# Kernel optimization log

Hardware: AMD Instinct MI355X
Metric: run time of the kernel (lower is better)

The kernel has to match this reference:

```python
import jax, jax.numpy as jnp
import numpy as np
import math

HEADS, LANDMARKS, PINV_ITERS, RES_K = 8, 256, 6, 33
DIM = 512


def layer_norm(x, g, b, eps=1e-5):
    mu = x.mean(-1, keepdims=True)
    var = ((x - mu) ** 2).mean(-1, keepdims=True)
    return (x - mu) * jax.lax.rsqrt(var + eps) * g + b


def iter_pinv(x, iters=PINV_ITERS):
    # Moore-Penrose pseudo-inverse via Newton-Schulz-like iteration (lucidrains nystrom-attention)
    ax = jnp.abs(x)
    z = jnp.swapaxes(x, -1, -2) / (jnp.max(ax.sum(-1)) * jnp.max(ax.sum(-2)))
    I = jnp.eye(x.shape[-1], dtype=x.dtype)
    for _ in range(iters):
        xz = x @ z
        z = 0.25 * z @ (13.0 * I - xz @ (15.0 * I - xz @ (7.0 * I - xz)))
    return z


def nystrom_attention(x, qkv_w, out_w, out_b, res_w):
    b, n, dim = x.shape
    h, m = HEADS, LANDMARKS
    d = dim // h
    pad = (m - n % m) % m
    xp = jnp.pad(x, ((0, 0), (pad, 0), (0, 0)))  # pad at sequence start (as in original)
    npad = n + pad
    qkv = xp @ qkv_w  # [b, npad, 3*dim]
    q, k, v = jnp.split(qkv, 3, axis=-1)
    q, k, v = (t.reshape(b, npad, h, d).transpose(0, 2, 1, 3) for t in (q, k, v))
    q = q * (d ** -0.5)
    l = npad // m
    q_l = q.reshape(b, h, m, l, d).mean(3)  # [b,h,m,d] landmarks
    k_l = k.reshape(b, h, m, l, d).mean(3)
    attn1 = jax.nn.softmax(jnp.einsum('bhid,bhjd->bhij', q, k_l), axis=-1)    # [b,h,npad,m]
    attn2 = jax.nn.softmax(jnp.einsum('bhid,bhjd->bhij', q_l, k_l), axis=-1)  # [b,h,m,m]
    attn3 = jax.nn.softmax(jnp.einsum('bhid,bhjd->bhij', q_l, k), axis=-1)    # [b,h,m,npad]
    out = (attn1 @ iter_pinv(attn2)) @ (attn3 @ v)  # [b,h,npad,d]
    # depthwise residual conv over sequence dim: v as NCHW = [b, heads, npad, d], kernel (33,1)
    res = jax.lax.conv_general_dilated(
        v, res_w, window_strides=(1, 1), padding=((RES_K // 2, RES_K // 2), (0, 0)),
        dimension_numbers=('NCHW', 'OIHW', 'NCHW'), feature_group_count=h)
    out = out + res
    out = out.transpose(0, 2, 1, 3).reshape(b, npad, dim)
    out = out @ out_w + out_b  # dropout is identity at eval
    return out[:, -n:]


def dwconv(x, w, b, k):
    y = jax.lax.conv_general_dilated(
        x, w, (1, 1), ((k // 2, k // 2), (k // 2, k // 2)),
        dimension_numbers=('NCHW', 'OIHW', 'NCHW'), feature_group_count=x.shape[1])
    return y + b[None, :, None, None]


def ppeg(x, H, W, w7, b7, w5, b5, w3, b3):
    B, _, C = x.shape
    cls_tok, feat = x[:, :1], x[:, 1:]
    cnn = feat.transpose(0, 2, 1).reshape(B, C, H, W)
    y = cnn + dwconv(cnn, w7, b7, 7) + dwconv(cnn, w5, b5, 5) + dwconv(cnn, w3, b3, 3)
    y = y.reshape(B, C, H * W).transpose(0, 2, 1)
    return jnp.concatenate([cls_tok, y], axis=1)


def _forward(features, fc1_w, fc1_b, cls_token,
             l1_norm_g, l1_norm_b, l1_qkv_w, l1_out_w, l1_out_b, l1_res_w,
             ppeg_w7, ppeg_b7, ppeg_w5, ppeg_b5, ppeg_w3, ppeg_b3,
             l2_norm_g, l2_norm_b, l2_qkv_w, l2_out_w, l2_out_b, l2_res_w,
             norm_g, norm_b, fc2_w, fc2_b):
    h = jax.nn.relu(features @ fc1_w + fc1_b)  # [B, N, 512]
    B, N, D = h.shape
    _H = _W = int(math.ceil(math.sqrt(N)))
    add_length = _H * _W - N
    h = jnp.concatenate([h, h[:, :add_length, :]], axis=1)  # square pad by wraparound
    h = jnp.concatenate([jnp.broadcast_to(cls_token, (B, 1, D)), h], axis=1)
    h = h + nystrom_attention(layer_norm(h, l1_norm_g, l1_norm_b), l1_qkv_w, l1_out_w, l1_out_b, l1_res_w)
    h = ppeg(h, _H, _W, ppeg_w7, ppeg_b7, ppeg_w5, ppeg_b5, ppeg_w3, ppeg_b3)
    h = h + nystrom_attention(layer_norm(h, l2_norm_g, l2_norm_b), l2_qkv_w, l2_out_w, l2_out_b, l2_res_w)
    h = layer_norm(h, norm_g, norm_b)[:, 0]
    return h @ fc2_w + fc2_b  # [B, num_classes]


def setup_inputs() -> dict:
    key = jax.random.key(0)
    ks = jax.random.split(key, 32)
    B, N, F, D = 2, 16000, 1024, DIM
    s = 0.02
    def rn(k, shape, scale=s):
        return jax.random.normal(k, shape, dtype=jnp.float32) * scale
    inp = {
        'features': jax.random.normal(ks[0], (B, N, F), dtype=jnp.float32),
        'fc1_w': rn(ks[1], (F, D)), 'fc1_b': jnp.zeros((D,), jnp.float32),
        'cls_token': rn(ks[2], (1, 1, D), 1.0),
        'l1_norm_g': jnp.ones((D,), jnp.float32), 'l1_norm_b': jnp.zeros((D,), jnp.float32),
        'l1_qkv_w': rn(ks[3], (D, 3 * D)),
        'l1_out_w': rn(ks[4], (D, D)), 'l1_out_b': jnp.zeros((D,), jnp.float32),
        'l1_res_w': rn(ks[5], (HEADS, 1, RES_K, 1)),
        'ppeg_w7': rn(ks[6], (D, 1, 7, 7)), 'ppeg_b7': jnp.zeros((D,), jnp.float32),
        'ppeg_w5': rn(ks[7], (D, 1, 5, 5)), 'ppeg_b5': jnp.zeros((D,), jnp.float32),
        'ppeg_w3': rn(ks[8], (D, 1, 3, 3)), 'ppeg_b3': jnp.zeros((D,), jnp.float32),
        'l2_norm_g': jnp.ones((D,), jnp.float32), 'l2_norm_b': jnp.zeros((D,), jnp.float32),
        'l2_qkv_w': rn(ks[9], (D, 3 * D)),
        'l2_out_w': rn(ks[10], (D, D)), 'l2_out_b': jnp.zeros((D,), jnp.float32),
        'l2_res_w': rn(ks[11], (HEADS, 1, RES_K, 1)),
        'norm_g': jnp.ones((D,), jnp.float32), 'norm_b': jnp.zeros((D,), jnp.float32),
        'fc2_w': rn(ks[12], (D, 1)), 'fc2_b': jnp.zeros((1,), jnp.float32),
    }
    return inp


def reference(features, fc1_w, fc1_b, cls_token,
              l1_norm_g, l1_norm_b, l1_qkv_w, l1_out_w, l1_out_b, l1_res_w,
              ppeg_w7, ppeg_b7, ppeg_w5, ppeg_b5, ppeg_w3, ppeg_b3,
              l2_norm_g, l2_norm_b, l2_qkv_w, l2_out_w, l2_out_b, l2_res_w,
              norm_g, norm_b, fc2_w, fc2_b):
    return _forward(features, fc1_w, fc1_b, cls_token,
                    l1_norm_g, l1_norm_b, l1_qkv_w, l1_out_w, l1_out_b, l1_res_w,
                    ppeg_w7, ppeg_b7, ppeg_w5, ppeg_b5, ppeg_w3, ppeg_b3,
                    l2_norm_g, l2_norm_b, l2_qkv_w, l2_out_w, l2_out_b, l2_res_w,
                    norm_g, norm_b, fc2_w, fc2_b)
```

## Files before the change

### kernel.cpp

```cpp
#include <hip/hip_runtime.h>
#include <math.h>

#define NTOK 16130
#define NPAD 16384
#define PADF 254
#define NB   2
#define DM   512
#define NH   8
#define HD   64
#define LM   256
#define SEG  64

typedef __attribute__((ext_vector_type(8))) short short8v;
typedef __attribute__((ext_vector_type(4))) float f32x4;
typedef unsigned int u32;

__device__ __forceinline__ float wred_max(float v){
  #pragma unroll
  for(int o=32;o;o>>=1) v=fmaxf(v,__shfl_xor(v,o));
  return v;
}
__device__ __forceinline__ float wred_sum(float v){
  #pragma unroll
  for(int o=32;o;o>>=1) v+=__shfl_xor(v,o);
  return v;
}
__device__ __forceinline__ float block_max256(float v, float* s4){
  v=wred_max(v);
  if((threadIdx.x&63)==0) s4[threadIdx.x>>6]=v;
  __syncthreads();
  v=fmaxf(fmaxf(s4[0],s4[1]),fmaxf(s4[2],s4[3]));
  __syncthreads();
  return v;
}
__device__ __forceinline__ float block_sum256(float v, float* s4){
  v=wred_sum(v);
  if((threadIdx.x&63)==0) s4[threadIdx.x>>6]=v;
  __syncthreads();
  v=s4[0]+s4[1]+s4[2]+s4[3];
  __syncthreads();
  return v;
}
__device__ __forceinline__ unsigned short f2bf(float f){
  unsigned u=__float_as_uint(f);
  u = u + 0x7FFFu + ((u>>16)&1u);
  return (unsigned short)(u>>16);
}
__device__ __forceinline__ float bf2f(unsigned short u){
  return __uint_as_float(((unsigned)u)<<16);
}
__device__ __forceinline__ unsigned cvtpk(float a, float b){
  unsigned r;
  asm("v_cvt_pk_bf16_f32 %0, %1, %2" : "=v"(r) : "v"(a), "v"(b));
  return r;
}
__device__ __forceinline__ void gl16(const unsigned short* g, unsigned short* l){
  __builtin_amdgcn_global_load_lds(
      (const __attribute__((address_space(1))) u32*)(g),
      (__attribute__((address_space(3))) u32*)(l), 16, 0, 0);
}

__global__ void k_f2bf4(const float* __restrict__ x, unsigned short* __restrict__ y, int n4){
  int i=blockIdx.x*256+threadIdx.x; if(i>=n4) return;
  float4 v=((const float4*)x)[i];
  ushort4 r; r.x=f2bf(v.x); r.y=f2bf(v.y); r.z=f2bf(v.z); r.w=f2bf(v.w);
  ((ushort4*)y)[i]=r;
}
__global__ void k_wconv_t(const float* __restrict__ W, unsigned short* __restrict__ Wt,
                          int K, int N){
  int idx=blockIdx.x*256+threadIdx.x; if(idx>=K*N) return;
  int k=idx/N, n=idx%N;
  Wt[(size_t)n*K+k]=f2bf(W[idx]);
}

template<int MODE, int ASRC>
__global__ __launch_bounds__(256) void k_mfma_gemm(
    const void* __restrict__ Ap, const unsigned short* __restrict__ Bt,
    int M, int N, int K,
    const float* __restrict__ bias,
    void* __restrict__ o0, void* __restrict__ o1, void* __restrict__ o2)
{
  __shared__ __align__(16) unsigned short Sh[128*64];
  int t=threadIdx.x;
  int bx=blockIdx.x, by=blockIdx.y;
  {
    int gx=gridDim.x; int wg=by*gx+bx; int nwg=gx*gridDim.y;
    int cpx=nwg>>3; int x2=(wg&7)*cpx+(wg>>3);
    by=x2/gx; bx=x2-by*gx;
  }
  int row0=by*128, col0=bx*128;
  int lane=t&63, w=t>>6, wr=w>>1, wc=w&1, lr=lane&15, kg=lane>>4;
  f32x4 acc[4][4];
  #pragma unroll
  for(int m=0;m<4;m++)
    #pragma unroll
    for(int n=0;n<4;n++) acc[m][n]=(f32x4){0.f,0.f,0.f,0.f};

  for(int k0=0;k0<K;k0+=32){
    __syncthreads();
    #pragma unroll
    for(int i=0;i<2;i++){
      int flat=i*256+t, r=flat>>2, k8=flat&3;
      int kofs=k0+k8*8;
      const unsigned short* asrc;
      if constexpr(ASRC==0){
        asrc=(const unsigned short*)Ap+(size_t)(row0+r)*K+kofs;
      } else {
        int rr2=row0+r; int bb=rr2>>14, ri=rr2&16383;
        int head=kofs>>6, dd=kofs&63;
        asrc=(const unsigned short*)Ap + (((size_t)bb*NH+head)*NPAD+ri)*HD + dd;
      }
      gl16(asrc, Sh+(size_t)flat*8);
      gl16(Bt+(size_t)(col0+r)*K+kofs, Sh+4096+(size_t)flat*8);
    }
    __syncthreads();
    short8v af[4], bf[4];
    #pragma unroll
    for(int m=0;m<4;m++) af[m]=*(const short8v*)(Sh+(wr*64+m*16+lr)*32 + kg*8);
    #pragma unroll
    for(int n=0;n<4;n++) bf[n]=*(const short8v*)(Sh+4096+(wc*64+n*16+lr)*32 + kg*8);
    #pragma unroll
    for(int m=0;m<4;m++)
      #pragma unroll
      for(int n=0;n<4;n++)
        acc[m][n]=__builtin_amdgcn_mfma_f32_16x16x32_bf16(af[m],bf[n],acc[m][n],0,0,0);
  }
  if constexpr(MODE==1){
    #pragma unroll
    for(int p=0;p<2;p++){
      __syncthreads();
      #pragma unroll
      for(int mm=0;mm<2;mm++){
        int m=2*p+mm;
        #pragma unroll
        for(int n=0;n<4;n++){
          int cc=wc*64+n*16+lr;
          int c=col0+cc;
          float sc=((c>>9)==0)?0.125f:1.f;
          #pragma unroll
          for(int j=0;j<4;j++){
            int lrow=wr*32+mm*16+kg*4+j;
            Sh[lrow*128+cc]=f2bf(acc[m][n][j]*sc);
          }
        }
      }
      __syncthreads();
      #pragma unroll
      for(int i=0;i<4;i++){
        int p2=i*256+t;
        int r2=p2>>4, ck=p2&15;
        int grow=row0+(r2>>5)*64+(2*p+((r2>>4)&1))*16+(r2&15);
        int bb=grow>>14, rr=grow&16383;
        int c=col0+ck*8;
        int which=c>>9, hcol=c&511, head=hcol>>6, dd=hcol&63;
        unsigned short* dst=(which==0)?(unsigned short*)o0:
                            (which==1)?(unsigned short*)o1:(unsigned short*)o2;
        *(short8v*)(dst + (((size_t)bb*NH+head)*NPAD+rr)*HD+dd) =
            *(const short8v*)(Sh + r2*128 + ck*8);
      }
    }
  } else {
    #pragma unroll
    for(int m=0;m<4;m++){
      int rbase=row0 + wr*64 + m*16 + kg*4;
      #pragma unroll
      for(int j=0;j<4;j++){
        int r=rbase+j;
        #pragma unroll
        for(int n=0;n<4;n++){
          int c=col0 + wc*64 + n*16 + lr;
          float val=acc[m][n][j];
          if(MODE==0){
            float* h=(float*)o0;
            int bb=(r>=16000)?1:0, ii=r-bb*16000;
            float vv=fmaxf(val+bias[c],0.f);
            h[((size_t)bb*NTOK + 1 + ii)*DM + c]=vv;
            if(ii<129) h[((size_t)bb*NTOK + 16001 + ii)*DM + c]=vv;
          } else {
            float* h=(float*)o0;
            int bb=r>>14, rr=r&16383;
            if(rr>=PADF)
              h[((size_t)bb*NTOK + (rr-PADF))*DM + c]+=val+bias[c];
          }
        }
      }
    }
  }
}

__global__ void k_cls(const float* __restrict__ cls, float* __restrict__ h){
  int t=blockIdx.x*256+threadIdx.x;
  if(t<2*DM) h[(size_t)(t>>9)*NTOK*DM + (t&511)]=cls[t&511];
}

__global__ __launch_bounds__(256) void k_lnpad(
    const float* __restrict__ h, const float* __restrict__ g,
    const float* __restrict__ bta, unsigned short* __restrict__ xln)
{
  int r=blockIdx.x;
  int bb=r>>14, i=r&16383;
  int t=threadIdx.x;
  unsigned short* dst=xln+(size_t)r*DM;
  if(i<PADF){ dst[t]=0; dst[t+256]=0; return; }
  const float* src=h+((size_t)bb*NTOK + (i-PADF))*DM;
  float x0=src[t], x1=src[t+256];
  __shared__ float s4[4];
  float mu=block_sum256(x0+x1,s4)*(1.f/512.f);
  float d0=x0-mu, d1=x1-mu;
  float var=block_sum256(d0*d0+d1*d1,s4)*(1.f/512.f);
  float rst=rsqrtf(var+1e-5f);
  dst[t]    =f2bf(d0*rst*g[t]    +bta[t]);
  dst[t+256]=f2bf(d1*rst*g[t+256]+bta[t+256]);
}

__global__ void k_lmean2(const unsigned short* __restrict__ qsrc,
                         const unsigned short* __restrict__ ksrc,
                         float* __restrict__ qlf, unsigned short* __restrict__ qlb_,
                         float* __restrict__ klf, unsigned short* __restrict__ klb_){
  int gid=blockIdx.x;
  const unsigned short* src; float* dstf; unsigned short* dstb;
  if(gid<4096){ src=qsrc; dstf=qlf; dstb=qlb_; }
  else        { src=ksrc; dstf=klf; dstb=klb_; gid-=4096; }
  int bh=gid>>8, s=gid&255, d=threadIdx.x;
  const unsigned short* p=src + (((size_t)bh*NPAD)+s*SEG)*HD + d;
  float acc=0.f;
  #pragma unroll
  for(int l=0;l<SEG;l++) acc+=bf2f(p[(size_t)l*HD]);
  float m=acc*(1.f/64.f);
  dstf[((size_t)bh*LM+s)*HD+d]=m;
  dstb[((size_t)bh*LM+s)*HD+d]=f2bf(m);
}

__global__ __launch_bounds__(256) void k_vtrans(
    const unsigned short* __restrict__ v, unsigned short* __restrict__ vt)
{
  __shared__ unsigned short tile[64][72];
  int kt=blockIdx.x, bh=blockIdx.y;
  int t=threadIdx.x;
  int r=t>>2, sgq=t&3;
  const short8v* src=(const short8v*)(v + ((size_t)bh*NPAD + kt*64 + r)*HD + sgq*16);
  *(short8v*)(&tile[r][sgq*16])  =src[0];
  *(short8v*)(&tile[r][sgq*16+8])=src[1];
  __syncthreads();
  int d=t>>2;
  union{unsigned short u[16]; short8v v8[2];} pk;
  #pragma unroll
  for(int i=0;i<16;i++) pk.u[i]=tile[sgq*16+i][d];
  short8v* dst=(short8v*)(vt + ((size_t)bh*HD + d)*NPAD + kt*64 + sgq*16);
  dst[0]=pk.v8[0]; dst[1]=pk.v8[1];
}

__global__ __launch_bounds__(256) void k_attn2(
    const float* __restrict__ ql, const float* __restrict__ kl,
    float* __restrict__ attn2,
    unsigned short* __restrict__ a2h, unsigned short* __restrict__ a2l)
{
  __shared__ float qrow[64]; __shared__ float s4[4];
  int bh=blockIdx.x>>8, i=blockIdx.x&255, j=threadIdx.x;
  if(j<64) qrow[j]=ql[((size_t)bh*LM+i)*HD+j];
  __syncthreads();
  const float* kp=kl+((size_t)bh*LM+j)*HD;
  float l=0.f;
  #pragma unroll
  for(int d=0;d<64;d++) l+=qrow[d]*kp[d];
  float m=block_max256(l,s4);
  float e=__expf(l-m);
  float s=block_sum256(e,s4);
  float pv=e/s;
  size_t o=((size_t)bh*LM+i)*LM+j;
  attn2[o]=pv;
  unsigned short hh=f2bf(pv);
  a2h[o]=hh; a2l[o]=f2bf(pv-bf2f(hh));
}

__global__ void k_colsum(const float* __restrict__ x, float* __restrict__ cs){
  int bh=blockIdx.x, j=threadIdx.x;
  const float* p=x+(size_t)bh*65536;
  float s=0.f;
  for(int i=0;i<256;i++) s+=p[(size_t)i*256+j];
  cs[bh*256+j]=s;
}
__global__ void k_pinvscale(const float* __restrict__ cs, float* __restrict__ scale){
  __shared__ float s4[4];
  float mc=-1e30f;
  for(int i=threadIdx.x;i<4096;i+=256) mc=fmaxf(mc,cs[i]);
  mc=block_max256(mc,s4);
  if(threadIdx.x==0) scale[0]=1.f/mc;
}
__global__ void k_zinit_hl(const float* __restrict__ x, const float* __restrict__ scale,
    unsigned short* __restrict__ zh, unsigned short* __restrict__ zl,
    unsigned short* __restrict__ zth, unsigned short* __restrict__ ztl){
  int bh=blockIdx.x>>8, i=blockIdx.x&255, j=threadIdx.x;
  float s=scale[0];
  size_t base=(size_t)bh*65536;
  float vn=x[base+(size_t)j*256+i]*s;
  float vt=x[base+(size_t)i*256+j]*s;
  size_t o=base+(size_t)i*256+j;
  unsigned short h=f2bf(vn); zh[o]=h; zl[o]=f2bf(vn-bf2f(h));
  h=f2bf(vt); zth[o]=h; ztl[o]=f2bf(vt-bf2f(h));
}

template<int MODE, int PREC>
__global__ __launch_bounds__(256) void k_bmm3(
    const unsigned short* __restrict__ Ah, const unsigned short* __restrict__ Al,
    const unsigned short* __restrict__ Bth, const unsigned short* __restrict__ Btl,
    const unsigned short* __restrict__ Xh, const unsigned short* __restrict__ Xl,
    unsigned short* __restrict__ Cnh, unsigned short* __restrict__ Cnl,
    unsigned short* __restrict__ Cth, unsigned short* __restrict__ Ctl,
    int Ndim)
{
  __shared__ unsigned short AsH[32*72], BsH[64*72];
  __shared__ unsigned short AsL[PREC?32*72:8], BsL[PREC?64*72:8];
  int bh=blockIdx.z;
  int n0=blockIdx.x*64, m0=blockIdx.y*32;
  int t=threadIdx.x, lane=t&63, w=t>>6;
  int c=lane&15, g=lane>>4;
  int wr=(w>>1)*16, wc=(w&1)*32;
  f32x4 acc[2];
  acc[0]=(f32x4){0.f,0.f,0.f,0.f};
  acc[1]=(f32x4){0.f,0.f,0.f,0.f};
  size_t Abase=(size_t)bh*65536;
  size_t Bbase=(size_t)bh*(size_t)Ndim*256;
  int r=t>>3, k8=(t&7)*8;
  const unsigned short* ApH =Ah +Abase+(size_t)(m0+r)*256+k8;
  const unsigned short* BpH0=Bth+Bbase+(size_t)(n0+r)*256+k8;
  const unsigned short* BpH1=Bth+Bbase+(size_t)(n0+32+r)*256+k8;
  const unsigned short* ApL =Al +Abase+(size_t)(m0+r)*256+k8;
  const unsigned short* BpL0=Btl+Bbase+(size_t)(n0+r)*256+k8;
  const unsigned short* BpL1=Btl+Bbase+(size_t)(n0+32+r)*256+k8;
  short8v rah,rbh0,rbh1, ral,rbl0,rbl1;
  rah =*(const short8v*)(ApH);
  rbh0=*(const short8v*)(BpH0);
  rbh1=*(const short8v*)(BpH1);
  if constexpr(PREC==1){
    ral =*(const short8v*)(ApL);
    rbl0=*(const short8v*)(BpL0);
    rbl1=*(const short8v*)(BpL1);
  }
  int k0=0;
  for(;;){
    __syncthreads();
    *(short8v*)(AsH + r*72 + k8)=rah;
    *(short8v*)(BsH + r*72 + k8)=rbh0;
    *(short8v*)(BsH + (r+32)*72 + k8)=rbh1;
    if constexpr(PREC==1){
      *(short8v*)(AsL + r*72 + k8)=ral;
      *(short8v*)(BsL + r*72 + k8)=rbl0;
      *(short8v*)(BsL + (r+32)*72 + k8)=rbl1;
    }
    __syncthreads();
    int kn=k0+64;
    if(kn<256){
      rah =*(const short8v*)(ApH +kn);
      rbh0=*(const short8v*)(BpH0+kn);
      rbh1=*(const short8v*)(BpH1+kn);
      if constexpr(PREC==1){
        ral =*(const short8v*)(ApL +kn);
        rbl0=*(const short8v*)(BpL0+kn);
        rbl1=*(const short8v*)(BpL1+kn);
      }
    }
    #pragma unroll
    for(int ks=0;ks<2;ks++){
      short8v af=*(const short8v*)(AsH+(wr+c)*72 + ks*32 + g*8);
      short8v alf;
      if constexpr(PREC==1) alf=*(const short8v*)(AsL+(wr+c)*72 + ks*32 + g*8);
      #pragma unroll
      for(int nt=0;nt<2;nt++){
        short8v bf=*(const short8v*)(BsH+(wc+nt*16+c)*72 + ks*32 + g*8);
        acc[nt]=__builtin_amdgcn_mfma_f32_16x16x32_bf16(af,bf,acc[nt],0,0,0);
        if constexpr(PREC==1){
          short8v blf=*(const short8v*)(BsL+(wc+nt*16+c)*72 + ks*32 + g*8);
          acc[nt]=__builtin_amdgcn_mfma_f32_16x16x32_bf16(af,blf,acc[nt],0,0,0);
          acc[nt]=__builtin_amdgcn_mfma_f32_16x16x32_bf16(alf,bf,acc[nt],0,0,0);
        }
      }
    }
    if(kn>=256) break;
    k0=kn;
  }
  int rb=m0+wr+g*4;
  #pragma unroll
  for(int nt=0;nt<2;nt++){
    int cc=n0+wc+nt*16+c;
    float vv[4];
    #pragma unroll
    for(int j=0;j<4;j++){
      float a=acc[nt][j];
      int rr=rb+j;
      if(MODE==1){
        float xv=bf2f(Xh[Abase+(size_t)rr*256+cc])+bf2f(Xl[Abase+(size_t)rr*256+cc]);
        a=(rr==cc?15.f:0.f)-7.f*xv+a;
      } else if(MODE==2){
        a=(rr==cc?13.f:0.f)-a;
      } else if(MODE==3){
        a*=0.25f;
      }
      vv[j]=a;
    }
    if(MODE==0||MODE==3){
      #pragma unroll
      for(int j=0;j<4;j++){
        unsigned short hh=f2bf(vv[j]);
        Cnh[Abase+(size_t)(rb+j)*256+cc]=hh;
        Cnl[Abase+(size_t)(rb+j)*256+cc]=f2bf(vv[j]-bf2f(hh));
      }
    }
    {
      ushort4 hv, lv;
      hv.x=f2bf(vv[0]); hv.y=f2bf(vv[1]); hv.z=f2bf(vv[2]); hv.w=f2bf(vv[3]);
      lv.x=f2bf(vv[0]-bf2f(hv.x)); lv.y=f2bf(vv[1]-bf2f(hv.y));
      lv.z=f2bf(vv[2]-bf2f(hv.z)); lv.w=f2bf(vv[3]-bf2f(hv.w));
      size_t co=((size_t)bh*Ndim+cc)*256+rb;
      *(ushort4*)(Cth+co)=hv;
      if(MODE!=4) *(ushort4*)(Ctl+co)=lv;
    }
  }
}

__global__ __launch_bounds__(512) void k_attn3m(
    const unsigned short* __restrict__ qlb,
    const unsigned short* __restrict__ kb,
    const unsigned short* __restrict__ vtb,
    float* __restrict__ pacc, float* __restrict__ pms)
{
  __shared__ unsigned short Ks[64*72];
  __shared__ unsigned short Vs[64*72];
  int ck=blockIdx.x, rh=blockIdx.y, bh=blockIdx.z;
  int t=threadIdx.x, lane=t&63, w=t>>6;
  int c=lane&15, g=lane>>4;
  int qrow0=rh*128 + w*16;
  short8v Qf[2];
  #pragma unroll
  for(int kw=0;kw<2;kw++)
    Qf[kw]=*(const short8v*)(qlb + ((size_t)bh*LM + qrow0 + c)*HD + kw*32 + g*8);
  f32x4 accO[4];
  float mrun=-3e38f, srun=0.f;
  #pragma unroll
  for(int d=0;d<4;d++) accO[d]=(f32x4){0.f,0.f,0.f,0.f};
  int sr=t>>3, sgk=t&7;
  for(int sc=0;sc<16;++sc){
    int key0=ck*1024 + sc*64;
    __syncthreads();
    *(short8v*)(Ks + sr*72 + sgk*8) =
      *(const short8v*)(kb + ((size_t)bh*NPAD + key0 + sr)*HD + sgk*8);
    *(short8v*)(Vs + sr*72 + sgk*8) =
      *(const short8v*)(vtb + ((size_t)bh*HD + sr)*NPAD + key0 + sgk*8);
    __syncthreads();
    f32x4 s[4];
    #pragma unroll
    for(int mt=0;mt<4;mt++){
      short8v a0=*(const short8v*)(Ks + (mt*16+c)*72 + g*8);
      short8v a1=*(const short8v*)(Ks + (mt*16+c)*72 + 32 + g*8);
      f32x4 z=(f32x4){0.f,0.f,0.f,0.f};
      z=__builtin_amdgcn_mfma_f32_16x16x32_bf16(a0,Qf[0],z,0,0,0);
      z=__builtin_amdgcn_mfma_f32_16x16x32_bf16(a1,Qf[1],z,0,0,0);
      s[mt]=z;
    }
    unsigned U[4][2];
    {
      float cm=-3e38f;
      #pragma unroll
      for(int mt=0;mt<4;mt++)
        #pragma unroll
        for(int j=0;j<4;j++) cm=fmaxf(cm,s[mt][j]);
      cm=fmaxf(cm,__shfl_xor(cm,16));
      cm=fmaxf(cm,__shfl_xor(cm,32));
      float mnew=fmaxf(mrun,cm);
      float f=__expf(mrun-mnew);
      mrun=mnew;
      float ps=0.f;
      #pragma unroll
      for(int mt=0;mt<4;mt++){
        float p0=__expf(s[mt][0]-mnew);
        float p1=__expf(s[mt][1]-mnew);
        float p2=__expf(s[mt][2]-mnew);
        float p3=__expf(s[mt][3]-mnew);
        ps+=p0+p1+p2+p3;
        U[mt][0]=cvtpk(p0,p1);
        U[mt][1]=cvtpk(p2,p3);
      }
      ps+=__shfl_xor(ps,16); ps+=__shfl_xor(ps,32);
      srun=srun*f+ps;
      #pragma unroll
      for(int d=0;d<4;d++){
        accO[d][0]*=f; accO[d][1]*=f; accO[d][2]*=f; accO[d][3]*=f;
      }
    }
    #pragma unroll
    for(int kw=0;kw<2;kw++){
      union{unsigned u[4]; short8v v;} pk;
      #pragma unroll
      for(int wd=0;wd<4;wd++){
        int sl=c+16*(((g&1)<<1)+(wd>>1));
        unsigned va=(unsigned)__shfl((int)U[kw*2  ][wd&1],sl);
        unsigned vb=(unsigned)__shfl((int)U[kw*2+1][wd&1],sl);
        pk.u[wd]=(lane>=32)?vb:va;
      }
      #pragma unroll
      for(int d=0;d<4;d++){
        short8v vf=*(const short8v*)(Vs + (d*16+c)*72 + kw*32 + g*8);
        accO[d]=__builtin_amdgcn_mfma_f32_16x16x32_bf16(vf,pk.v,accO[d],0,0,0);
      }
    }
  }
  size_t pb=((size_t)bh*16+ck)*LM;
  int q=qrow0+c;
  #pragma unroll
  for(int d=0;d<4;d++)
    *(f32x4*)(pacc + (pb+q)*HD + d*16 + g*4)=accO[d];
  if(g==0){ pms[(pb+q)*2]=mrun; pms[(pb+q)*2+1]=srun; }
}
__global__ __launch_bounds__(256) void k_attn3vc(
    const float* __restrict__ pacc, const float* __restrict__ pms,
    unsigned short* __restrict__ a3vth, unsigned short* __restrict__ a3vtl)
{
  int gid=blockIdx.x*4+(threadIdx.x>>6);
  int bh=gid>>8, row=gid&255, lane=threadIdx.x&63;
  float M=-3e38f;
  float ms[16], ss[16];
  #pragma unroll
  for(int c=0;c<16;c++){
    size_t pb=((size_t)bh*16+c)*LM+row;
    ms[c]=pms[pb*2]; ss[c]=pms[pb*2+1];
    M=fmaxf(M,ms[c]);
  }
  float S=0.f,a=0.f;
  #pragma unroll
  for(int c=0;c<16;c++){
    float f=__expf(ms[c]-M);
    S+=ss[c]*f;
    a+=pacc[(((size_t)bh*16+c)*LM+row)*HD+lane]*f;
  }
  float v=a/S;
  unsigned short hi=f2bf(v);
  a3vth[((size_t)bh*HD+lane)*LM+row]=hi;
  a3vtl[((size_t)bh*HD+lane)*LM+row]=f2bf(v-bf2f(hi));
}

__global__ __launch_bounds__(512) void k_attn1m(
    const unsigned short* __restrict__ qb,
    const unsigned short* __restrict__ klb,
    const unsigned short* __restrict__ w2t,
    unsigned short* __restrict__ aohb)
{
  __shared__ unsigned short klS[256*72];
  __shared__ unsigned short w2S[64*264];
  int qt=blockIdx.x, bh=blockIdx.y;
  int t=threadIdx.x, lane=t&63, w=t>>6;
  int c=lane&15, g=lane>>4;
  {
    int r=t>>1, hf=t&1;
    const short8v* s=(const short8v*)(klb + ((size_t)bh*LM+r)*HD + hf*32);
    short8v* d=(short8v*)(klS + r*72 + hf*32);
    d[0]=s[0]; d[1]=s[1]; d[2]=s[2]; d[3]=s[3];
    int r2=t>>3, sg2=t&7;
    const short8v* s2=(const short8v*)(w2t + ((size_t)bh*HD+r2)*LM + sg2*32);
    short8v* d2=(short8v*)(w2S + r2*264 + sg2*32);
    d2[0]=s2[0]; d2[1]=s2[1]; d2[2]=s2[2]; d2[3]=s2[3];
  }
  __syncthreads();
  int q0=qt*256 + w*32;
  #pragma unroll
  for(int n=0;n<2;n++){
    const unsigned short* qrow=qb + ((size_t)bh*NPAD + q0 + n*16 + c)*HD;
    short8v qf0=*(const short8v*)(qrow + g*8);
    short8v qf1=*(const short8v*)(qrow + 32 + g*8);
    f32x4 s[16];
    #pragma unroll
    for(int mt=0;mt<16;mt++){
      short8v a0=*(const short8v*)(klS + (mt*16+c)*72 + g*8);
      short8v a1=*(const short8v*)(klS + (mt*16+c)*72 + 32 + g*8);
      f32x4 z=(f32x4){0.f,0.f,0.f,0.f};
      z=__builtin_amdgcn_mfma_f32_16x16x32_bf16(a0,qf0,z,0,0,0);
      z=__builtin_amdgcn_mfma_f32_16x16x32_bf16(a1,qf1,z,0,0,0);
      s[mt]=z;
    }
    float M=-3e38f;
    #pragma unroll
    for(int mt=0;mt<16;mt++)
      #pragma unroll
      for(int j=0;j<4;j++) M=fmaxf(M,s[mt][j]);
    M=fmaxf(M,__shfl_xor(M,16));
    M=fmaxf(M,__shfl_xor(M,32));
    float sum=0.f;
    unsigned U[16][2];
    #pragma unroll
    for(int mt=0;mt<16;mt++){
      float p0=__expf(s[mt][0]-M);
      float p1=__expf(s[mt][1]-M);
      float p2=__expf(s[mt][2]-M);
      float p3=__expf(s[mt][3]-M);
      sum+=p0+p1+p2+p3;
      U[mt][0]=cvtpk(p0,p1);
      U[mt][1]=cvtpk(p2,p3);
    }
    sum+=__shfl_xor(sum,16); sum+=__shfl_xor(sum,32);
    float inv=1.f/sum;
    f32x4 accO[4];
    #pragma unroll
    for(int d=0;d<4;d++) accO[d]=(f32x4){0.f,0.f,0.f,0.f};
    #pragma unroll
    for(int kw=0;kw<8;kw++){
      union{unsigned u[4]; short8v v;} pk;
      #pragma unroll
      for(int wd=0;wd<4;wd++){
        int sl=c+16*(((g&1)<<1)+(wd>>1));
        unsigned va=(unsigned)__shfl((int)U[kw*2  ][wd&1],sl);
        unsigned vb=(unsigned)__shfl((int)U[kw*2+1][wd&1],sl);
        pk.u[wd]=(lane>=32)?vb:va;
      }
      #pragma unroll
      for(int d=0;d<4;d++){
        short8v vf=*(const short8v*)(w2S + (d*16+c)*264 + kw*32 + g*8);
        accO[d]=__builtin_amdgcn_mfma_f32_16x16x32_bf16(vf,pk.v,accO[d],0,0,0);
      }
    }
    int q=q0+n*16+c;
    #pragma unroll
    for(int d=0;d<4;d++){
      f32x4 o=accO[d];
      uint2 pk2;
      pk2.x=cvtpk(o[0]*inv, o[1]*inv);
      pk2.y=cvtpk(o[2]*inv, o[3]*inv);
      *(uint2*)(aohb + ((size_t)bh*NPAD+q)*HD + d*16 + g*4)=pk2;
    }
  }
}

__global__ __launch_bounds__(256) void k_resconv2(
    const unsigned short* __restrict__ vt, const float* __restrict__ rw,
    unsigned short* __restrict__ aohb){
  int bx=blockIdx.x, bh=blockIdx.y;
  int t=threadIdx.x, d=t&63, g=t>>6;
  int i0=bx*32+g*8;
  int hh=bh&7;
  const unsigned short* vr=vt + ((size_t)bh*HD + d)*NPAD;
  float wv[40];
  int start=i0-16;
  if(start>=0 && start+40<=NPAD){
    #pragma unroll
    for(int b=0;b<5;b++){
      short8v v8=*(const short8v*)(vr+start+b*8);
      #pragma unroll
      for(int j=0;j<8;j++) wv[b*8+j]=bf2f((unsigned short)v8[j]);
    }
  } else {
    #pragma unroll
    for(int t2=0;t2<40;t2++){
      int src=start+t2;
      wv[t2]=(src>=0&&src<NPAD)?bf2f(vr[src]):0.f;
    }
  }
  const float* wt=rw+hh*33;
  #pragma unroll
  for(int p=0;p<8;p++){
    float a=0.f;
    #pragma unroll
    for(int tk=0;tk<33;tk++) a+=wv[p+tk]*wt[tk];
    size_t o=((size_t)bh*NPAD+i0+p)*HD+d;
    aohb[o]=f2bf(bf2f(aohb[o])+a);
  }
}

__global__ void k_wprep(const float* __restrict__ w7, const float* __restrict__ b7,
                        const float* __restrict__ w5, const float* __restrict__ b5,
                        const float* __restrict__ w3, const float* __restrict__ b3,
                        unsigned short* __restrict__ wcat){
  int t=blockIdx.x*256+threadIdx.x;
  if(t>=50*512) return;
  int r=t>>9, c=t&511;
  float v;
  if(r<49){
    int ky=r/7, kx=r%7;
    v=w7[(size_t)c*49+r];
    if(ky>=1&&ky<=5&&kx>=1&&kx<=5) v+=w5[(size_t)c*25+(ky-1)*5+(kx-1)];
    if(ky>=2&&ky<=4&&kx>=2&&kx<=4) v+=w3[(size_t)c*9+(ky-2)*3+(kx-2)];
  } else {
    v=b7[c]+b5[c]+b3[c];
  }
  wcat[t]=f2bf(v);
}

__global__ __launch_bounds__(256,4) void k_ppeg4(
    const float* __restrict__ src, const unsigned short* __restrict__ wcat,
    float* __restrict__ dst)
{
  __shared__ float patch[196][32];
  __shared__ float wsf[50][32];
  int bx=blockIdx.x;
  int cz=blockIdx.y, bb=blockIdx.z;
  int t=threadIdx.x, c=t&31, g=t>>5;
  int ty0=(bx>>4)*8, tx0=(bx&15)*8;
  const float* base=src+((size_t)bb*NTOK+1)*DM + cz*32 + c;
  #pragma unroll
  for(int i=0;i<25;i++){
    int p=g+8*i;
    if(p<196){
      int py=p/14, px=p%14;
      int yy=ty0-3+py, xx=tx0-3+px;
      float v=0.f;
      if(yy>=0&&yy<127&&xx>=0&&xx<127) v=base[(size_t)(yy*127+xx)*DM];
      patch[p][c]=v;
    }
  }
  #pragma unroll
  for(int i=0;i<7;i++){
    int r=g+8*i; if(r<50) wsf[r][c]=bf2f(wcat[(size_t)r*DM + cz*32 + c]);
  }
  __syncthreads();
  float acc[8];
  float bias=wsf[49][c];
  #pragma unroll
  for(int j=0;j<8;j++) acc[j]=patch[(g+3)*14+(j+3)][c]+bias;
  #pragma unroll
  for(int ky=0;ky<7;ky++){
    float win[14];
    #pragma unroll
    for(int x=0;x<14;x++) win[x]=patch[(g+ky)*14+x][c];
    #pragma unroll
    for(int kx=0;kx<7;kx++){
      float wv=wsf[ky*7+kx][c];
      #pragma unroll
      for(int j=0;j<8;j++) acc[j]+=win[j+kx]*wv;
    }
  }
  int y=ty0+g;
  if(y<127){
    #pragma unroll
    for(int j=0;j<8;j++){
      int x=tx0+j;
      if(x<127)
        dst[((size_t)bb*NTOK+1+(size_t)(y*127+x))*DM + cz*32 + c]=acc[j];
    }
  }
}

__global__ void k_cpcls(const float* __restrict__ h, float* __restrict__ dst){
  int t=blockIdx.x*256+threadIdx.x;
  if(t<2*DM) dst[(size_t)(t>>9)*NTOK*DM + (t&511)]=h[(size_t)(t>>9)*NTOK*DM + (t&511)];
}

__global__ __launch_bounds__(256) void k_final(
    const float* __restrict__ h, const float* __restrict__ g, const float* __restrict__ bta,
    const float* __restrict__ w, const float* __restrict__ fb, float* __restrict__ out)
{
  int bb=blockIdx.x, t=threadIdx.x;
  const float* src=h+(size_t)bb*NTOK*DM;
  float x0=src[t], x1=src[t+256];
  __shared__ float s4[4];
  float mu=block_sum256(x0+x1,s4)*(1.f/512.f);
  float d0=x0-mu, d1=x1-mu;
  float var=block_sum256(d0*d0+d1*d1,s4)*(1.f/512.f);
  float rst=rsqrtf(var+1e-5f);
  float y0=d0*rst*g[t]+bta[t], y1=d1*rst*g[t+256]+bta[t+256];
  float dot=block_sum256(y0*w[t]+y1*w[t+256],s4);
  if(t==0) out[bb]=dot+fb[0];
}

extern "C" void kernel_launch(void* const* d_in, const int* in_sizes, int n_in,
                              void* d_out, int out_size, void* d_ws, size_t ws_size,
                              hipStream_t stream){
  (void)in_sizes; (void)n_in; (void)out_size; (void)ws_size;
  const float* features=(const float*)d_in[0];
  const float* fc1_w  =(const float*)d_in[1];
  const float* fc1_b  =(const float*)d_in[2];
  const float* cls_tok=(const float*)d_in[3];
  const float* fc2_w  =(const float*)d_in[24];
  const float* fc2_b  =(const float*)d_in[25];
  float* out=(float*)d_out;

  char* wp=(char*)d_ws;
  auto allocB=[&](size_t bytes)->char*{
    char* p=wp; wp+=((bytes+255)/256)*256; return p;
  };
  float* h    =(float*)allocB((size_t)NB*NTOK*DM*4);
  float* h2   =(float*)allocB((size_t)NB*NTOK*DM*4);
  unsigned short* vb  =(unsigned short*)allocB((size_t)NB*NPAD*DM*2);
  unsigned short* xlnb=(unsigned short*)allocB((size_t)NB*NPAD*DM*2);
  unsigned short* qb  =(unsigned short*)allocB((size_t)NB*NPAD*DM*2);
  unsigned short* kb  =(unsigned short*)allocB((size_t)NB*NPAD*DM*2);
  unsigned short* vtb =(unsigned short*)allocB((size_t)NB*NPAD*DM*2);
  unsigned short* aohb=(unsigned short*)allocB((size_t)NB*NPAD*DM*2);
  unsigned short* wtf=(unsigned short*)allocB((size_t)512*1024*2);
  unsigned short* wtq=(unsigned short*)allocB((size_t)1536*512*2);
  unsigned short* wtp=(unsigned short*)allocB((size_t)512*512*2);
  float* ql =(float*)allocB((size_t)16*LM*HD*4);
  float* kl =(float*)allocB((size_t)16*LM*HD*4);
  unsigned short* qlb=(unsigned short*)allocB((size_t)16*LM*HD*2);
  unsigned short* klb=(unsigned short*)allocB((size_t)16*LM*HD*2);
  float* attn2=(float*)allocB((size_t)16*LM*LM*4);
  unsigned short* a2h=(unsigned short*)allocB((size_t)16*LM*LM*2);
  unsigned short* a2l=(unsigned short*)allocB((size_t)16*LM*LM*2);
  unsigned short* zb[8];
  for(int i=0;i<8;i++) zb[i]=(unsigned short*)allocB((size_t)16*LM*LM*2);
  unsigned short* Abh=(unsigned short*)allocB((size_t)16*LM*LM*2);
  unsigned short* Abl=(unsigned short*)allocB((size_t)16*LM*LM*2);
  unsigned short* Abth=(unsigned short*)allocB((size_t)16*LM*LM*2);
  unsigned short* Abtl=(unsigned short*)allocB((size_t)16*LM*LM*2);
  unsigned short* Ubth=(unsigned short*)allocB((size_t)16*LM*LM*2);
  unsigned short* Ubtl=(unsigned short*)allocB((size_t)16*LM*LM*2);
  unsigned short* Tbth=(unsigned short*)allocB((size_t)16*LM*LM*2);
  unsigned short* Tbtl=(unsigned short*)allocB((size_t)16*LM*LM*2);
  unsigned short* a3vth=(unsigned short*)allocB((size_t)16*HD*LM*2);
  unsigned short* a3vtl=(unsigned short*)allocB((size_t)16*HD*LM*2);
  unsigned short* w2t=(unsigned short*)allocB((size_t)16*HD*LM*2);
  float* pacc=(float*)allocB((size_t)16*16*LM*HD*4);
  float* pms =(float*)allocB((size_t)16*16*LM*2*4);
  float* cs  =(float*)allocB(4096*4);
  float* scl =(float*)allocB(64*4);

  auto nystrom=[&](float* hbuf, const float* ng, const float* nbias, const float* qkvw,
                   const float* outw, const float* outb, const float* resw){
    k_lnpad<<<NB*NPAD,256,0,stream>>>(hbuf, ng, nbias, xlnb);
    k_wconv_t<<<(512*1536+255)/256,256,0,stream>>>(qkvw, wtq, 512, 1536);
    k_mfma_gemm<1,0><<<dim3(12,256),256,0,stream>>>(xlnb, wtq, 32768,1536,512,
                                                    nullptr, qb, kb, vb);
    k_lmean2<<<8192,64,0,stream>>>(qb, kb, ql, qlb, kl, klb);
    k_vtrans<<<dim3(256,16),256,0,stream>>>(vb, vtb);
    k_attn2<<<4096,256,0,stream>>>(ql, kl, attn2, a2h, a2l);
    k_colsum<<<16,256,0,stream>>>(attn2, cs);
    k_pinvscale<<<1,256,0,stream>>>(cs, scl);
    k_zinit_hl<<<4096,256,0,stream>>>(attn2, scl, zb[0],zb[1],zb[2],zb[3]);
    unsigned short *zch=zb[0],*zcl=zb[1],*zcth=zb[2],*zctl=zb[3];
    unsigned short *znh=zb[4],*znl=zb[5],*znth=zb[6],*zntl=zb[7];
    for(int it=0;it<6;it++){
      if(it<5){
        k_bmm3<0,0><<<dim3(4,8,16),256,0,stream>>>(a2h,a2l, zcth,zctl, nullptr,nullptr,
                                                   Abh,Abl, Abth,Abtl, 256);
        k_bmm3<1,0><<<dim3(4,8,16),256,0,stream>>>(Abh,Abl, Abth,Abtl, Abh,Abl,
                                                   nullptr,nullptr, Ubth,Ubtl, 256);
        k_bmm3<2,0><<<dim3(4,8,16),256,0,stream>>>(Abh,Abl, Ubth,Ubtl, nullptr,nullptr,
                                                   nullptr,nullptr, Tbth,Tbtl, 256);
        k_bmm3<3,0><<<dim3(4,8,16),256,0,stream>>>(zch,zcl, Tbth,Tbtl, nullptr,nullptr,
                                                   znh,znl, znth,zntl, 256);
      } else {
        k_bmm3<0,1><<<dim3(4,8,16),256,0,stream>>>(a2h,a2l, zcth,zctl, nullptr,nullptr,
                                                   Abh,Abl, Abth,Abtl, 256);
        k_bmm3<1,1><<<dim3(4,8,16),256,0,stream>>>(Abh,Abl, Abth,Abtl, Abh,Abl,
                                                   nullptr,nullptr, Ubth,Ubtl, 256);
        k_bmm3<2,1><<<dim3(4,8,16),256,0,stream>>>(Abh,Abl, Ubth,Ubtl, nullptr,nullptr,
                                                   nullptr,nullptr, Tbth,Tbtl, 256);
        k_bmm3<3,1><<<dim3(4,8,16),256,0,stream>>>(zch,zcl, Tbth,Tbtl, nullptr,nullptr,
                                                   znh,znl, znth,zntl, 256);
      }
      unsigned short* tp;
      tp=zch; zch=znh; znh=tp;  tp=zcl; zcl=znl; znl=tp;
      tp=zcth; zcth=znth; znth=tp;  tp=zctl; zctl=zntl; zntl=tp;
    }
    k_attn3m<<<dim3(16,2,16),512,0,stream>>>(qlb, kb, vtb, pacc, pms);
    k_attn3vc<<<1024,256,0,stream>>>(pacc, pms, a3vth, a3vtl);
    k_bmm3<4,1><<<dim3(1,8,16),256,0,stream>>>(zch,zcl, a3vth,a3vtl, nullptr,nullptr,
                                               nullptr,nullptr, w2t,nullptr, 64);
    k_attn1m<<<dim3(64,16),512,0,stream>>>(qb, klb, w2t, aohb);
    k_resconv2<<<dim3(512,16),256,0,stream>>>(vtb, resw, aohb);
    k_wconv_t<<<(512*512+255)/256,256,0,stream>>>(outw, wtp, 512, 512);
    k_mfma_gemm<2,3><<<dim3(4,256),256,0,stream>>>(aohb, wtp, 32768,512,512,
                                                   outb, hbuf, nullptr, nullptr);
  };

  unsigned short* featbf=(unsigned short*)h2;
  k_f2bf4<<<32000,256,0,stream>>>(features, featbf, 32000*1024/4);
  k_wconv_t<<<(1024*512+255)/256,256,0,stream>>>(fc1_w, wtf, 1024, 512);
  k_mfma_gemm<0,0><<<dim3(4,250),256,0,stream>>>(featbf, wtf, 32000,512,1024,
                                                 fc1_b, h, nullptr, nullptr);
  k_cls<<<4,256,0,stream>>>(cls_tok, h);

  nystrom(h, (const float*)d_in[4],(const float*)d_in[5],(const float*)d_in[6],
          (const float*)d_in[7],(const float*)d_in[8],(const float*)d_in[9]);

  {
    unsigned short* wcat=(unsigned short*)attn2;
    k_wprep<<<100,256,0,stream>>>(
        (const float*)d_in[10],(const float*)d_in[11],
        (const float*)d_in[12],(const float*)d_in[13],
        (const float*)d_in[14],(const float*)d_in[15], wcat);
    k_cpcls<<<4,256,0,stream>>>(h, h2);
    k_ppeg4<<<dim3(256,16,2),256,0,stream>>>(h, wcat, h2);
  }

  nystrom(h2, (const float*)d_in[16],(const float*)d_in[17],(const float*)d_in[18],
          (const float*)d_in[19],(const float*)d_in[20],(const float*)d_in[21]);

  k_final<<<2,256,0,stream>>>(h2,(const float*)d_in[22],(const float*)d_in[23],
                              fc2_w, fc2_b, out);
}
```

Measured before the change: 1.264 ms.

## Vectorize and tile several small helper kernels for coalesced memory access

The weight transpose-convert kernel and the pinv initialisation now go through a 32x32 shared-memory tile, so both global reads and writes are coalesced and vectorised. LayerNorm-with-padding handles one row per wavefront with float4 loads and wave-shuffle reductions instead of block-wide reductions. The column sum over attn2 is split into two stages so more blocks run in parallel, and it reuses the pacc buffer as scratch. These kernels were strided-access or low-occupancy helpers; the change adds launches and shared-memory syncs in exchange.

```diff
diff --git a/kernel.cpp b/kernel.cpp
--- a/kernel.cpp
+++ b/kernel.cpp
@@ -66,11 +66,18 @@
   ushort4 r; r.x=f2bf(v.x); r.y=f2bf(v.y); r.z=f2bf(v.z); r.w=f2bf(v.w);
   ((ushort4*)y)[i]=r;
 }
-__global__ void k_wconv_t(const float* __restrict__ W, unsigned short* __restrict__ Wt,
-                          int K, int N){
-  int idx=blockIdx.x*256+threadIdx.x; if(idx>=K*N) return;
-  int k=idx/N, n=idx%N;
-  Wt[(size_t)n*K+k]=f2bf(W[idx]);
+__global__ __launch_bounds__(256) void k_wconv_t(
+    const float* __restrict__ W, unsigned short* __restrict__ Wt, int K, int N){
+  __shared__ float T[32][33];
+  int k0=blockIdx.x*32, n0=blockIdx.y*32;
+  int t=threadIdx.x, r=t>>3, c4=(t&7)*4;
+  float4 a=*(const float4*)(W+(size_t)(k0+r)*N + n0+c4);
+  T[r][c4]=a.x; T[r][c4+1]=a.y; T[r][c4+2]=a.z; T[r][c4+3]=a.w;
+  __syncthreads();
+  ushort4 w;
+  w.x=f2bf(T[c4+0][r]); w.y=f2bf(T[c4+1][r]);
+  w.z=f2bf(T[c4+2][r]); w.w=f2bf(T[c4+3][r]);
+  *(ushort4*)(Wt+(size_t)(n0+r)*K + k0+c4)=w;
 }
 
 template<int MODE, int ASRC>
@@ -197,20 +204,37 @@
     const float* __restrict__ h, const float* __restrict__ g,
     const float* __restrict__ bta, unsigned short* __restrict__ xln)
 {
-  int r=blockIdx.x;
-  int bb=r>>14, i=r&16383;
-  int t=threadIdx.x;
-  unsigned short* dst=xln+(size_t)r*DM;
-  if(i<PADF){ dst[t]=0; dst[t+256]=0; return; }
-  const float* src=h+((size_t)bb*NTOK + (i-PADF))*DM;
-  float x0=src[t], x1=src[t+256];
-  __shared__ float s4[4];
-  float mu=block_sum256(x0+x1,s4)*(1.f/512.f);
-  float d0=x0-mu, d1=x1-mu;
-  float var=block_sum256(d0*d0+d1*d1,s4)*(1.f/512.f);
-  float rst=rsqrtf(var+1e-5f);
-  dst[t]    =f2bf(d0*rst*g[t]    +bta[t]);
-  dst[t+256]=f2bf(d1*rst*g[t+256]+bta[t+256]);
+  int wid=blockIdx.x*4+(threadIdx.x>>6);
+  int lane=threadIdx.x&63;
+  int bb=wid>>14, i=wid&16383;
+  unsigned short* dst=xln+(size_t)wid*DM+lane*8;
+  if(i<PADF){
+    ushort4 z=(ushort4){0,0,0,0};
+    *(ushort4*)dst=z; *(ushort4*)(dst+4)=z;
+    return;
+  }
+  const float* src=h+((size_t)bb*NTOK + (i-PADF))*DM + lane*8;
+  float4 v0=*(const float4*)src;
+  float4 v1=*(const float4*)(src+4);
+  float x[8]={v0.x,v0.y,v0.z,v0.w,v1.x,v1.y,v1.z,v1.w};
+  float s=0.f;
+  #pragma unroll
+  for(int k=0;k<8;k++) s+=x[k];
+  float mu=wred_sum(s)*(1.f/512.f);
+  float d[8]; float vs=0.f;
+  #pragma unroll
+  for(int k=0;k<8;k++){ d[k]=x[k]-mu; vs+=d[k]*d[k]; }
+  float rst=rsqrtf(wred_sum(vs)*(1.f/512.f)+1e-5f);
+  float4 g0=*(const float4*)(g+lane*8),   g1=*(const float4*)(g+lane*8+4);
+  float4 b0=*(const float4*)(bta+lane*8), b1=*(const float4*)(bta+lane*8+4);
+  float gg[8]={g0.x,g0.y,g0.z,g0.w,g1.x,g1.y,g1.z,g1.w};
+  float bb8[8]={b0.x,b0.y,b0.z,b0.w,b1.x,b1.y,b1.z,b1.w};
+  ushort4 w0,w1;
+  w0.x=f2bf(d[0]*rst*gg[0]+bb8[0]); w0.y=f2bf(d[1]*rst*gg[1]+bb8[1]);
+  w0.z=f2bf(d[2]*rst*gg[2]+bb8[2]); w0.w=f2bf(d[3]*rst*gg[3]+bb8[3]);
+  w1.x=f2bf(d[4]*rst*gg[4]+bb8[4]); w1.y=f2bf(d[5]*rst*gg[5]+bb8[5]);
+  w1.z=f2bf(d[6]*rst*gg[6]+bb8[6]); w1.w=f2bf(d[7]*rst*gg[7]+bb8[7]);
+  *(ushort4*)dst=w0; *(ushort4*)(dst+4)=w1;
 }
 
 __global__ void k_lmean2(const unsigned short* __restrict__ qsrc,
@@ -273,11 +297,19 @@
   a2h[o]=hh; a2l[o]=f2bf(pv-bf2f(hh));
 }
 
-__global__ void k_colsum(const float* __restrict__ x, float* __restrict__ cs){
+__global__ void k_colsumA(const float* __restrict__ x, float* __restrict__ partial){
+  int bh=blockIdx.y, ic=blockIdx.x, j=threadIdx.x;
+  const float* p=x+(size_t)bh*65536+(size_t)ic*16*256;
+  float s=0.f;
+  #pragma unroll
+  for(int i=0;i<16;i++) s+=p[(size_t)i*256+j];
+  partial[((size_t)bh*16+ic)*256+j]=s;
+}
+__global__ void k_colsumB(const float* __restrict__ partial, float* __restrict__ cs){
   int bh=blockIdx.x, j=threadIdx.x;
-  const float* p=x+(size_t)bh*65536;
   float s=0.f;
-  for(int i=0;i<256;i++) s+=p[(size_t)i*256+j];
+  #pragma unroll
+  for(int ic=0;ic<16;ic++) s+=partial[((size_t)bh*16+ic)*256+j];
   cs[bh*256+j]=s;
 }
 __global__ void k_pinvscale(const float* __restrict__ cs, float* __restrict__ scale){
@@ -287,17 +319,36 @@
   mc=block_max256(mc,s4);
   if(threadIdx.x==0) scale[0]=1.f/mc;
 }
-__global__ void k_zinit_hl(const float* __restrict__ x, const float* __restrict__ scale,
+__global__ __launch_bounds__(256) void k_zinit_hl(
+    const float* __restrict__ x, const float* __restrict__ scale,
     unsigned short* __restrict__ zh, unsigned short* __restrict__ zl,
     unsigned short* __restrict__ zth, unsigned short* __restrict__ ztl){
-  int bh=blockIdx.x>>8, i=blockIdx.x&255, j=threadIdx.x;
+  __shared__ float T1[32][33], T2[32][33];
+  int bh=blockIdx.x>>6, tile=blockIdx.x&63;
+  int i0=(tile>>3)*32, j0=(tile&7)*32;
+  int t=threadIdx.x, r=t>>3, c4=(t&7)*4;
+  size_t base=(size_t)bh*65536;
+  float4 a=*(const float4*)(x+base+(size_t)(i0+r)*256+j0+c4);
+  float4 b=*(const float4*)(x+base+(size_t)(j0+r)*256+i0+c4);
+  T1[r][c4]=a.x; T1[r][c4+1]=a.y; T1[r][c4+2]=a.z; T1[r][c4+3]=a.w;
+  T2[r][c4]=b.x; T2[r][c4+1]=b.y; T2[r][c4+2]=b.z; T2[r][c4+3]=b.w;
+  __syncthreads();
   float s=scale[0];
-  size_t base=(size_t)bh*65536;
-  float vn=x[base+(size_t)j*256+i]*s;
-  float vt=x[base+(size_t)i*256+j]*s;
-  size_t o=base+(size_t)i*256+j;
-  unsigned short h=f2bf(vn); zh[o]=h; zl[o]=f2bf(vn-bf2f(h));
-  h=f2bf(vt); zth[o]=h; ztl[o]=f2bf(vt-bf2f(h));
+  size_t o=base+(size_t)(i0+r)*256+j0+c4;
+  ushort4 nh,nl,th,tl;
+  {
+    float vn, vt; unsigned short hh;
+    vn=T2[c4+0][r]*s; hh=f2bf(vn); nh.x=hh; nl.x=f2bf(vn-bf2f(hh));
+    vn=T2[c4+1][r]*s; hh=f2bf(vn); nh.y=hh; nl.y=f2bf(vn-bf2f(hh));
+    vn=T2[c4+2][r]*s; hh=f2bf(vn); nh.z=hh; nl.z=f2bf(vn-bf2f(hh));
+    vn=T2[c4+3][r]*s; hh=f2bf(vn); nh.w=hh; nl.w=f2bf(vn-bf2f(hh));
+    vt=T1[r][c4+0]*s; hh=f2bf(vt); th.x=hh; tl.x=f2bf(vt-bf2f(hh));
+    vt=T1[r][c4+1]*s; hh=f2bf(vt); th.y=hh; tl.y=f2bf(vt-bf2f(hh));
+    vt=T1[r][c4+2]*s; hh=f2bf(vt); th.z=hh; tl.z=f2bf(vt-bf2f(hh));
+    vt=T1[r][c4+3]*s; hh=f2bf(vt); th.w=hh; tl.w=f2bf(vt-bf2f(hh));
+  }
+  *(ushort4*)(zh+o)=nh; *(ushort4*)(zl+o)=nl;
+  *(ushort4*)(zth+o)=th; *(ushort4*)(ztl+o)=tl;
 }
 
 template<int MODE, int PREC>
@@ -812,16 +863,17 @@
 
   auto nystrom=[&](float* hbuf, const float* ng, const float* nbias, const float* qkvw,
                    const float* outw, const float* outb, const float* resw){
-    k_lnpad<<<NB*NPAD,256,0,stream>>>(hbuf, ng, nbias, xlnb);
-    k_wconv_t<<<(512*1536+255)/256,256,0,stream>>>(qkvw, wtq, 512, 1536);
+    k_lnpad<<<NB*NPAD/4,256,0,stream>>>(hbuf, ng, nbias, xlnb);
+    k_wconv_t<<<dim3(16,48),256,0,stream>>>(qkvw, wtq, 512, 1536);
     k_mfma_gemm<1,0><<<dim3(12,256),256,0,stream>>>(xlnb, wtq, 32768,1536,512,
                                                     nullptr, qb, kb, vb);
     k_lmean2<<<8192,64,0,stream>>>(qb, kb, ql, qlb, kl, klb);
     k_vtrans<<<dim3(256,16),256,0,stream>>>(vb, vtb);
     k_attn2<<<4096,256,0,stream>>>(ql, kl, attn2, a2h, a2l);
-    k_colsum<<<16,256,0,stream>>>(attn2, cs);
+    k_colsumA<<<dim3(16,16),256,0,stream>>>(attn2, pacc);
+    k_colsumB<<<16,256,0,stream>>>(pacc, cs);
     k_pinvscale<<<1,256,0,stream>>>(cs, scl);
-    k_zinit_hl<<<4096,256,0,stream>>>(attn2, scl, zb[0],zb[1],zb[2],zb[3]);
+    k_zinit_hl<<<1024,256,0,stream>>>(attn2, scl, zb[0],zb[1],zb[2],zb[3]);
     unsigned short *zch=zb[0],*zcl=zb[1],*zcth=zb[2],*zctl=zb[3];
     unsigned short *znh=zb[4],*znl=zb[5],*znth=zb[6],*zntl=zb[7];
     for(int it=0;it<6;it++){
@@ -854,14 +906,14 @@
                                                nullptr,nullptr, w2t,nullptr, 64);
     k_attn1m<<<dim3(64,16),512,0,stream>>>(qb, klb, w2t, aohb);
     k_resconv2<<<dim3(512,16),256,0,stream>>>(vtb, resw, aohb);
-    k_wconv_t<<<(512*512+255)/256,256,0,stream>>>(outw, wtp, 512, 512);
+    k_wconv_t<<<dim3(16,16),256,0,stream>>>(outw, wtp, 512, 512);
     k_mfma_gemm<2,3><<<dim3(4,256),256,0,stream>>>(aohb, wtp, 32768,512,512,
                                                    outb, hbuf, nullptr, nullptr);
   };
 
   unsigned short* featbf=(unsigned short*)h2;
   k_f2bf4<<<32000,256,0,stream>>>(features, featbf, 32000*1024/4);
-  k_wconv_t<<<(1024*512+255)/256,256,0,stream>>>(fc1_w, wtf, 1024, 512);
+  k_wconv_t<<<dim3(32,16),256,0,stream>>>(fc1_w, wtf, 1024, 512);
   k_mfma_gemm<0,0><<<dim3(4,250),256,0,stream>>>(featbf, wtf, 32000,512,1024,
                                                  fc1_b, h, nullptr, nullptr);
   k_cls<<<4,256,0,stream>>>(cls_tok, h);
```

Measured after the change: 1.207 ms. 4.5% less time.
